# Kernel tuning notes

Hardware: AMD Instinct MI355X
Metric: run time of the kernel (lower is better)

Reference implementation:

```python
import jax, jax.numpy as jnp
import numpy as np

B, S, H = 2, 2048, 1024
I = 1024          # moe_intermediate_size
E = 8             # n_routed_experts
K = 2             # num_experts_per_tok
SCALE = 1.0       # routed_scaling_factor


def setup_inputs() -> dict:
    key = jax.random.key(0)
    ks = jax.random.split(key, 8)
    sd = 1.0 / np.sqrt(H)
    si = 1.0 / np.sqrt(I)
    return {
        "hidden_states": jax.random.normal(ks[0], (B, S, H), jnp.float32),
        "router_w": jax.random.uniform(ks[1], (E, H), jnp.float32, -sd, sd),
        # shared expert (n_shared_experts = 1); weights stored [in, out]
        "shared_gate": jax.random.uniform(ks[2], (H, I), jnp.float32, -sd, sd),
        "shared_up": jax.random.uniform(ks[3], (H, I), jnp.float32, -sd, sd),
        "shared_down": jax.random.uniform(ks[4], (I, H), jnp.float32, -si, si),
        # routed experts, stacked [E, in, out]
        "experts_gate": jax.random.uniform(ks[5], (E, H, I), jnp.float32, -sd, sd),
        "experts_up": jax.random.uniform(ks[6], (E, H, I), jnp.float32, -sd, sd),
        "experts_down": jax.random.uniform(ks[7], (E, I, H), jnp.float32, -si, si),
    }


def reference(hidden_states, router_w, shared_gate, shared_up, shared_down,
              experts_gate, experts_up, experts_down):
    residual = hidden_states
    x = hidden_states.reshape(-1, H)                      # [T, H], T = B*S

    # shared expert (SwiGLU-ish: sigmoid(gate) * up)
    sg = x @ shared_gate
    su = x @ shared_up
    shared_out = (jax.nn.sigmoid(sg) * su) @ shared_down  # [T, H]

    # router: softmax over experts, greedy top-k
    logits = x @ router_w.T                               # [T, E]
    scores = jax.nn.softmax(logits.astype(jnp.float32), axis=-1)
    topk_w, topk_idx = jax.lax.top_k(scores, K)           # [T, K]
    topk_w = topk_w * SCALE

    # dense compute of ALL experts on all tokens (faithful to reference)
    g = jnp.einsum('th,ehi->tei', x, experts_gate)        # [T, E, I]
    u = jnp.einsum('th,ehi->tei', x, experts_up)
    hid = jax.nn.sigmoid(g) * u
    expert_outputs = jnp.einsum('tei,eih->teh', hid, experts_down)  # [T, E, H]

    # gather top-k expert outputs and combine
    selected = jnp.take_along_axis(expert_outputs, topk_idx[:, :, None], axis=1)  # [T, K, H]
    routed_out = (selected * topk_w[:, :, None]).sum(axis=1)                      # [T, H]

    out = residual + (shared_out + routed_out).reshape(B, S, H)
    return out
```

## Files before the change

### kernel.cpp

```cpp
#include <hip/hip_runtime.h>
#include <hip/hip_bf16.h>

#define T_TOK 4096
#define HDIM 1024
#define IDIM 1024
#define EDIM 8
#define HID_SHARED_BASE 8320

typedef __attribute__((ext_vector_type(8))) short bf16x8;
typedef __attribute__((ext_vector_type(4))) float f32x4;

static __device__ __forceinline__ unsigned short f2bf(float f) {
  union { float f; unsigned int u; } v; v.f = f;
  unsigned int u = v.u;
  unsigned int r = u + 0x7FFFu + ((u >> 16) & 1u);
  return (unsigned short)(r >> 16);
}

#define GLD16(g, l) __builtin_amdgcn_global_load_lds( \
    (const __attribute__((address_space(1))) void*)(g), \
    (__attribute__((address_space(3))) void*)(l), 16, 0, 0)

__global__ __launch_bounds__(256) void convert_x(const float4* __restrict__ x4,
                                                 ushort4* __restrict__ xb4,
                                                 float4* __restrict__ out4) {
  int i = blockIdx.x * 256 + threadIdx.x;
  float4 v = x4[i];
  out4[i] = v;
  ushort4 o;
  o.x = f2bf(v.x); o.y = f2bf(v.y); o.z = f2bf(v.z); o.w = f2bf(v.w);
  xb4[i] = o;
}

__global__ void zero_cnt(int* __restrict__ cnt) {
  if (threadIdx.x < 16) cnt[threadIdx.x] = 0;
}

struct SrcPtrs { const float* p[6]; };

__global__ __launch_bounds__(256) void transpose_all(SrcPtrs S,
                                                     unsigned short* __restrict__ dstBase) {
  __shared__ unsigned short t[64][72];
  const int z = blockIdx.z;
  const float* src; int dz;
  if (z == 0)      { src = S.p[0];                              dz = 8;  }
  else if (z == 1) { src = S.p[1];                              dz = 17; }
  else if (z == 2) { src = S.p[2];                              dz = 26; }
  else if (z < 11) { src = S.p[3] + (size_t)(z - 3)  * 1048576; dz = z - 3; }
  else if (z < 19) { src = S.p[4] + (size_t)(z - 11) * 1048576; dz = 9 + (z - 11); }
  else             { src = S.p[5] + (size_t)(z - 19) * 1048576; dz = 18 + (z - 19); }
  unsigned short* dst = dstBase + (size_t)dz * 1048576;

  const int r0 = blockIdx.y * 64;
  const int c0 = blockIdx.x * 64;
  const int tid = threadIdx.x;

  const int rr = tid >> 4;
  const int c4 = (tid & 15) * 4;
#pragma unroll
  for (int ph = 0; ph < 4; ph++) {
    const int r = rr + ph * 16;
    const float4 v = *(const float4*)&src[(size_t)(r0 + r) * 1024 + c0 + c4];
    const int cs = c4 ^ (4 * (r >> 3));
    t[r][cs + 0] = f2bf(v.x); t[r][cs + 1] = f2bf(v.y);
    t[r][cs + 2] = f2bf(v.z); t[r][cs + 3] = f2bf(v.w);
  }
  __syncthreads();

  const int n = tid >> 3;
  const int k8 = (tid & 7) * 8;
  const int m = k8 >> 3;
#pragma unroll
  for (int ph = 0; ph < 2; ph++) {
    const int nn = n + ph * 32;
    const int ns = nn ^ (4 * m);
    unsigned short v[8];
#pragma unroll
    for (int j = 0; j < 8; j++) v[j] = t[k8 + j][ns];
    *(bf16x8*)&dst[(size_t)(c0 + nn) * 1024 + r0 + k8] = *(const bf16x8*)v;
  }
}

__global__ __launch_bounds__(256) void router2(
    const float* __restrict__ x, const float* __restrict__ rw,
    int* __restrict__ cnt, int* __restrict__ list, float* __restrict__ wgt) {
  __shared__ float rwT[1024 * 8];
  const int tid = threadIdx.x;
#pragma unroll
  for (int c = 0; c < 4; c++) {
    const int h = c * 256 + tid;
    float v[8];
#pragma unroll
    for (int e = 0; e < EDIM; e++) v[e] = rw[e * 1024 + h];
    *(float4*)&rwT[h * 8]     = make_float4(v[0], v[1], v[2], v[3]);
    *(float4*)&rwT[h * 8 + 4] = make_float4(v[4], v[5], v[6], v[7]);
  }
  __syncthreads();

  const int tt = tid >> 4;
  const int pp = tid & 15;
  const int t = blockIdx.x * 16 + tt;
  const float* xr = x + (size_t)t * HDIM;

  float a[EDIM];
#pragma unroll
  for (int e = 0; e < EDIM; e++) a[e] = 0.f;

#pragma unroll 8
  for (int i = 0; i < 64; i++) {
    const int h = pp + 16 * i;
    const float xs = xr[h];
    const float4 r0 = *(const float4*)&rwT[h * 8];
    const float4 r1 = *(const float4*)&rwT[h * 8 + 4];
    a[0] += xs * r0.x; a[1] += xs * r0.y; a[2] += xs * r0.z; a[3] += xs * r0.w;
    a[4] += xs * r1.x; a[5] += xs * r1.y; a[6] += xs * r1.z; a[7] += xs * r1.w;
  }
#pragma unroll
  for (int s = 1; s < 16; s <<= 1) {
#pragma unroll
    for (int e = 0; e < EDIM; e++) a[e] += __shfl_xor(a[e], s, 16);
  }
  if (pp == 0) {
    float m = a[0];
#pragma unroll
    for (int e = 1; e < EDIM; e++) m = fmaxf(m, a[e]);
    float p[EDIM]; float s = 0.f;
#pragma unroll
    for (int e = 0; e < EDIM; e++) { p[e] = expf(a[e] - m); s += p[e]; }
    float inv = 1.f / s;
    int e1 = 0; float b1 = p[0];
#pragma unroll
    for (int e = 1; e < EDIM; e++) if (p[e] > b1) { b1 = p[e]; e1 = e; }
    int e2 = -1; float b2 = -1.f;
#pragma unroll
    for (int e = 0; e < EDIM; e++) if (e != e1 && p[e] > b2) { b2 = p[e]; e2 = e; }
    int pos1 = atomicAdd(&cnt[e1], 1);
    list[e1 * T_TOK + pos1] = t; wgt[e1 * T_TOK + pos1] = b1 * inv;
    int pos2 = atomicAdd(&cnt[e2], 1);
    list[e2 * T_TOK + pos2] = t; wgt[e2 * T_TOK + pos2] = b2 * inv;
  }
}

__global__ __launch_bounds__(256) void gateup_f(
    const unsigned short* __restrict__ xb,
    const unsigned short* __restrict__ gateT,
    const unsigned short* __restrict__ upT,
    unsigned short* __restrict__ hid,
    const int* __restrict__ cnt, const int* __restrict__ list) {
  __shared__ unsigned short Al[3][128 * 32];
  __shared__ unsigned short Bg[3][64 * 32];
  __shared__ unsigned short Bu[3][64 * 32];

  const int tid = threadIdx.x;
  const int lane = tid & 63;
  const int w = tid >> 6;
  const int wm = w >> 1, wn = w & 1;
  const int z = blockIdx.z;
  const int m0 = blockIdx.y * 128;
  const int n0 = blockIdx.x * 64;

  int count, hidbase;
  if (z < EDIM) {
    count = cnt[z];
    if (m0 >= count) return;
    int off = 0;
#pragma unroll
    for (int i = 0; i < EDIM; i++) off += (i < z) ? cnt[i] : 0;
    hidbase = off;
  } else {
    count = T_TOK;
    hidbase = HID_SHARED_BASE;
  }
  const unsigned short* wg = gateT + (size_t)z * HDIM * IDIM;
  const unsigned short* wu = upT   + (size_t)z * HDIM * IDIM;

  const unsigned short* gA[2];
#pragma unroll
  for (int j = 0; j < 2; j++) {
    const int s = w * 128 + j * 64 + lane;
    const int row = s >> 2;
    const int g = (s & 3) ^ ((row + (row >> 2)) & 3);
    int tok;
    if (z < EDIM) {
      int p = m0 + row; if (p >= count) p = count - 1;
      tok = list[z * T_TOK + p];
    } else tok = m0 + row;
    gA[j] = xb + (size_t)tok * HDIM + g * 8;
  }
  const int sB = w * 64 + lane;
  const int rowB = sB >> 2;
  const int gB = (sB & 3) ^ ((rowB + (rowB >> 2)) & 3);
  const unsigned short* gGp = wg + (size_t)(n0 + rowB) * HDIM + gB * 8;
  const unsigned short* gUp = wu + (size_t)(n0 + rowB) * HDIM + gB * 8;

  f32x4 accg[4][2], accu[4][2];
  const f32x4 z4 = {0.f, 0.f, 0.f, 0.f};
#pragma unroll
  for (int i = 0; i < 4; i++)
#pragma unroll
    for (int j = 0; j < 2; j++) { accg[i][j] = z4; accu[i][j] = z4; }

  const int q = lane >> 4;
  const int r16 = lane & 15;
  const int ch = (q ^ ((r16 + (r16 >> 2)) & 3)) * 8;

  auto stage = [&](int k0, int b) {
    GLD16(gA[0] + k0, &Al[b][(w * 128) * 8]);
    GLD16(gA[1] + k0, &Al[b][(w * 128 + 64) * 8]);
    GLD16(gGp + k0, &Bg[b][(w * 64) * 8]);
    GLD16(gUp + k0, &Bu[b][(w * 64) * 8]);
  };
  auto compute = [&](int b) {
    bf16x8 af[4], bg2[2], bu2[2];
#pragma unroll
    for (int i = 0; i < 4; i++)
      af[i] = *(const bf16x8*)&Al[b][(wm * 64 + i * 16 + r16) * 32 + ch];
#pragma unroll
    for (int j = 0; j < 2; j++) {
      bg2[j] = *(const bf16x8*)&Bg[b][(wn * 32 + j * 16 + r16) * 32 + ch];
      bu2[j] = *(const bf16x8*)&Bu[b][(wn * 32 + j * 16 + r16) * 32 + ch];
    }
#pragma unroll
    for (int i = 0; i < 4; i++)
#pragma unroll
      for (int j = 0; j < 2; j++) {
        accg[i][j] = __builtin_amdgcn_mfma_f32_16x16x32_bf16(af[i], bg2[j], accg[i][j], 0, 0, 0);
        accu[i][j] = __builtin_amdgcn_mfma_f32_16x16x32_bf16(af[i], bu2[j], accu[i][j], 0, 0, 0);
      }
  };

  stage(0, 0);
  stage(32, 1);
#pragma unroll 1
  for (int p = 0; p < 32; p++) {
    if (p < 30) {
      asm volatile("s_waitcnt vmcnt(4)" ::: "memory");
    } else {
      asm volatile("s_waitcnt vmcnt(0)" ::: "memory");
    }
    __builtin_amdgcn_s_barrier();
    if (p + 2 < 32) stage((p + 2) * 32, (p + 2) % 3);
    compute(p % 3);
  }

#pragma unroll
  for (int i = 0; i < 4; i++) {
#pragma unroll
    for (int j = 0; j < 2; j++) {
      const int col = n0 + wn * 32 + j * 16 + r16;
#pragma unroll
      for (int r = 0; r < 4; r++) {
        int pos = m0 + wm * 64 + i * 16 + q * 4 + r;
        if (pos < count) {
          float g = accg[i][j][r], u = accu[i][j][r];
          float h = u / (1.f + __expf(-g));
          hid[(size_t)(hidbase + pos) * IDIM + col] = f2bf(h);
        }
      }
    }
  }
}

__global__ __launch_bounds__(256) void down_f(
    const unsigned short* __restrict__ hid,
    const unsigned short* __restrict__ downT,
    float* __restrict__ out,
    const int* __restrict__ cnt, const int* __restrict__ list,
    const float* __restrict__ wgt) {
  __shared__ unsigned short Al[3][128 * 32];
  __shared__ unsigned short Bl[3][128 * 32];

  const int tid = threadIdx.x;
  const int lane = tid & 63;
  const int w = tid >> 6;
  const int wm = w >> 1, wn = w & 1;
  const int z = blockIdx.z;
  const int m0 = blockIdx.y * 128;
  const int n0 = blockIdx.x * 128;

  int count, abase;
  if (z < EDIM) {
    count = cnt[z];
    if (m0 >= count) return;
    int off = 0;
#pragma unroll
    for (int i = 0; i < EDIM; i++) off += (i < z) ? cnt[i] : 0;
    abase = off;
  } else {
    count = T_TOK;
    abase = HID_SHARED_BASE;
  }
  const unsigned short* wd = downT + (size_t)z * IDIM * HDIM;

  const unsigned short *gA[2], *gBp[2];
#pragma unroll
  for (int j = 0; j < 2; j++) {
    const int s = w * 128 + j * 64 + lane;
    const int row = s >> 2;
    const int g = (s & 3) ^ ((row + (row >> 2)) & 3);
    gA[j]  = hid + (size_t)(abase + m0 + row) * IDIM + g * 8;
    gBp[j] = wd + (size_t)(n0 + row) * IDIM + g * 8;
  }

  f32x4 acc[4][4];
  const f32x4 z4 = {0.f, 0.f, 0.f, 0.f};
#pragma unroll
  for (int i = 0; i < 4; i++)
#pragma unroll
    for (int j = 0; j < 4; j++) acc[i][j] = z4;

  const int q = lane >> 4;
  const int r16 = lane & 15;
  const int ch = (q ^ ((r16 + (r16 >> 2)) & 3)) * 8;

  auto stage = [&](int k0, int b) {
    GLD16(gA[0] + k0,  &Al[b][(w * 128) * 8]);
    GLD16(gA[1] + k0,  &Al[b][(w * 128 + 64) * 8]);
    GLD16(gBp[0] + k0, &Bl[b][(w * 128) * 8]);
    GLD16(gBp[1] + k0, &Bl[b][(w * 128 + 64) * 8]);
  };
  auto compute = [&](int b) {
    bf16x8 af[4], bf4[4];
#pragma unroll
    for (int i = 0; i < 4; i++)
      af[i] = *(const bf16x8*)&Al[b][(wm * 64 + i * 16 + r16) * 32 + ch];
#pragma unroll
    for (int j = 0; j < 4; j++)
      bf4[j] = *(const bf16x8*)&Bl[b][(wn * 64 + j * 16 + r16) * 32 + ch];
#pragma unroll
    for (int i = 0; i < 4; i++)
#pragma unroll
      for (int j = 0; j < 4; j++)
        acc[i][j] = __builtin_amdgcn_mfma_f32_16x16x32_bf16(af[i], bf4[j], acc[i][j], 0, 0, 0);
  };

  stage(0, 0);
  stage(32, 1);
#pragma unroll 1
  for (int p = 0; p < 32; p++) {
    if (p < 30) {
      asm volatile("s_waitcnt vmcnt(4)" ::: "memory");
    } else {
      asm volatile("s_waitcnt vmcnt(0)" ::: "memory");
    }
    __builtin_amdgcn_s_barrier();
    if (p + 2 < 32) stage((p + 2) * 32, (p + 2) % 3);
    compute(p % 3);
  }

#pragma unroll
  for (int i = 0; i < 4; i++) {
    int toks[4]; float ws4[4];
#pragma unroll
    for (int r = 0; r < 4; r++) {
      int pos = m0 + wm * 64 + i * 16 + q * 4 + r;
      if (z < EDIM) {
        bool ok = pos < count;
        toks[r] = ok ? list[z * T_TOK + pos] : -1;
        ws4[r] = ok ? wgt[z * T_TOK + pos] : 0.f;
      } else {
        toks[r] = pos; ws4[r] = 1.f;
      }
    }
#pragma unroll
    for (int j = 0; j < 4; j++) {
      const int col = n0 + wn * 64 + j * 16 + r16;
#pragma unroll
      for (int r = 0; r < 4; r++) {
        if (toks[r] >= 0)
          atomicAdd(&out[(size_t)toks[r] * HDIM + col], ws4[r] * acc[i][j][r]);
      }
    }
  }
}

extern "C" void kernel_launch(void* const* d_in, const int* in_sizes, int n_in,
                              void* d_out, int out_size, void* d_ws, size_t ws_size,
                              hipStream_t stream) {
  const float* x  = (const float*)d_in[0];
  const float* rw = (const float*)d_in[1];
  const float* sg = (const float*)d_in[2];
  const float* su = (const float*)d_in[3];
  const float* sd = (const float*)d_in[4];
  const float* eg = (const float*)d_in[5];
  const float* eu = (const float*)d_in[6];
  const float* ed = (const float*)d_in[7];
  float* out = (float*)d_out;

  char* ws = (char*)d_ws;
  unsigned short* xb  = (unsigned short*)ws;
  unsigned short* hid = xb + (size_t)T_TOK * HDIM;
  int*   cnt  = (int*)(hid + (size_t)(HID_SHARED_BASE + T_TOK) * IDIM);
  int*   list = cnt + 16;
  float* wgt  = (float*)(list + EDIM * T_TOK);
  unsigned short* wT    = (unsigned short*)(wgt + EDIM * T_TOK);
  unsigned short* gateT = wT;
  unsigned short* upT   = wT + (size_t)9 * 1048576;
  unsigned short* downT = wT + (size_t)18 * 1048576;

  zero_cnt<<<1, 64, 0, stream>>>(cnt);
  convert_x<<<(T_TOK * HDIM) / 1024, 256, 0, stream>>>(
      (const float4*)x, (ushort4*)xb, (float4*)out);
  router2<<<T_TOK / 16, 256, 0, stream>>>(x, rw, cnt, list, wgt);

  SrcPtrs S; S.p[0] = sg; S.p[1] = su; S.p[2] = sd; S.p[3] = eg; S.p[4] = eu; S.p[5] = ed;
  transpose_all<<<dim3(16, 16, 27), 256, 0, stream>>>(S, wT);

  gateup_f<<<dim3(IDIM / 64, 32, 9), 256, 0, stream>>>(xb, gateT, upT, hid, cnt, list);
  down_f<<<dim3(HDIM / 128, 32, 9), 256, 0, stream>>>(hid, downT, out, cnt, list, wgt);
}
```

Measured before the change: 378.5 us.

## Replace atomic output accumulation with bf16 staging buffer, register transpose, fused zeroing

Adds a workspace buffer R with three bf16 slots per token (two routed experts plus the shared expert). down_f writes its weighted results there instead of issuing float atomicAdds into the output, and a new combine kernel sums the slots with the residual. The weight transpose now works in registers without shared memory, and zeroing the counters is folded into convert_x so one launch is dropped. This removes atomic contention and the extra output initialisation pass, at the cost of bf16 rounding of partial outputs, extra memory traffic for R, and a dependence on the workspace being large enough.

```diff
diff --git a/kernel.cpp b/kernel.cpp
--- a/kernel.cpp
+++ b/kernel.cpp
@@ -16,6 +16,10 @@
   unsigned int r = u + 0x7FFFu + ((u >> 16) & 1u);
   return (unsigned short)(r >> 16);
 }
+static __device__ __forceinline__ float bf2f(unsigned short s) {
+  union { unsigned int u; float f; } v; v.u = ((unsigned int)s) << 16;
+  return v.f;
+}
 
 #define GLD16(g, l) __builtin_amdgcn_global_load_lds( \
     (const __attribute__((address_space(1))) void*)(g), \
@@ -23,24 +27,21 @@
 
 __global__ __launch_bounds__(256) void convert_x(const float4* __restrict__ x4,
                                                  ushort4* __restrict__ xb4,
-                                                 float4* __restrict__ out4) {
+                                                 float4* __restrict__ out4,
+                                                 int* __restrict__ cnt, int initOut) {
   int i = blockIdx.x * 256 + threadIdx.x;
+  if (blockIdx.x == 0 && threadIdx.x < 16) cnt[threadIdx.x] = 0;
   float4 v = x4[i];
-  out4[i] = v;
+  if (initOut) out4[i] = v;
   ushort4 o;
   o.x = f2bf(v.x); o.y = f2bf(v.y); o.z = f2bf(v.z); o.w = f2bf(v.w);
   xb4[i] = o;
 }
 
-__global__ void zero_cnt(int* __restrict__ cnt) {
-  if (threadIdx.x < 16) cnt[threadIdx.x] = 0;
-}
-
 struct SrcPtrs { const float* p[6]; };
 
 __global__ __launch_bounds__(256) void transpose_all(SrcPtrs S,
                                                      unsigned short* __restrict__ dstBase) {
-  __shared__ unsigned short t[64][72];
   const int z = blockIdx.z;
   const float* src; int dz;
   if (z == 0)      { src = S.p[0];                              dz = 8;  }
@@ -51,33 +52,25 @@
   else             { src = S.p[5] + (size_t)(z - 19) * 1048576; dz = 18 + (z - 19); }
   unsigned short* dst = dstBase + (size_t)dz * 1048576;
 
-  const int r0 = blockIdx.y * 64;
-  const int c0 = blockIdx.x * 64;
   const int tid = threadIdx.x;
-
-  const int rr = tid >> 4;
-  const int c4 = (tid & 15) * 4;
-#pragma unroll
-  for (int ph = 0; ph < 4; ph++) {
-    const int r = rr + ph * 16;
-    const float4 v = *(const float4*)&src[(size_t)(r0 + r) * 1024 + c0 + c4];
-    const int cs = c4 ^ (4 * (r >> 3));
-    t[r][cs + 0] = f2bf(v.x); t[r][cs + 1] = f2bf(v.y);
-    t[r][cs + 2] = f2bf(v.z); t[r][cs + 3] = f2bf(v.w);
-  }
-  __syncthreads();
-
-  const int n = tid >> 3;
-  const int k8 = (tid & 7) * 8;
-  const int m = k8 >> 3;
-#pragma unroll
-  for (int ph = 0; ph < 2; ph++) {
-    const int nn = n + ph * 32;
-    const int ns = nn ^ (4 * m);
-    unsigned short v[8];
-#pragma unroll
-    for (int j = 0; j < 8; j++) v[j] = t[k8 + j][ns];
-    *(bf16x8*)&dst[(size_t)(c0 + nn) * 1024 + r0 + k8] = *(const bf16x8*)v;
+  const int rid = tid & 7;
+  const int cid = tid >> 3;
+  const int r = blockIdx.y * 64 + rid * 8;
+  const int c = blockIdx.x * 128 + cid * 4;
+
+  float4 v[8];
+#pragma unroll
+  for (int i = 0; i < 8; i++)
+    v[i] = *(const float4*)&src[(size_t)(r + i) * 1024 + c];
+
+#pragma unroll
+  for (int j = 0; j < 4; j++) {
+    unsigned short o[8];
+    o[0] = f2bf(v[0][j]); o[1] = f2bf(v[1][j]);
+    o[2] = f2bf(v[2][j]); o[3] = f2bf(v[3][j]);
+    o[4] = f2bf(v[4][j]); o[5] = f2bf(v[5][j]);
+    o[6] = f2bf(v[6][j]); o[7] = f2bf(v[7][j]);
+    *(bf16x8*)&dst[(size_t)(c + j) * 1024 + r] = *(const bf16x8*)o;
   }
 }
 
@@ -135,9 +128,9 @@
 #pragma unroll
     for (int e = 0; e < EDIM; e++) if (e != e1 && p[e] > b2) { b2 = p[e]; e2 = e; }
     int pos1 = atomicAdd(&cnt[e1], 1);
-    list[e1 * T_TOK + pos1] = t; wgt[e1 * T_TOK + pos1] = b1 * inv;
+    list[e1 * T_TOK + pos1] = (t << 1);      wgt[e1 * T_TOK + pos1] = b1 * inv;
     int pos2 = atomicAdd(&cnt[e2], 1);
-    list[e2 * T_TOK + pos2] = t; wgt[e2 * T_TOK + pos2] = b2 * inv;
+    list[e2 * T_TOK + pos2] = (t << 1) | 1;  wgt[e2 * T_TOK + pos2] = b2 * inv;
   }
 }
 
@@ -183,7 +176,7 @@
     int tok;
     if (z < EDIM) {
       int p = m0 + row; if (p >= count) p = count - 1;
-      tok = list[z * T_TOK + p];
+      tok = list[z * T_TOK + p] >> 1;
     } else tok = m0 + row;
     gA[j] = xb + (size_t)tok * HDIM + g * 8;
   }
@@ -264,7 +257,7 @@
 __global__ __launch_bounds__(256) void down_f(
     const unsigned short* __restrict__ hid,
     const unsigned short* __restrict__ downT,
-    float* __restrict__ out,
+    float* __restrict__ out, unsigned short* __restrict__ R, int useR,
     const int* __restrict__ cnt, const int* __restrict__ list,
     const float* __restrict__ wgt) {
   __shared__ unsigned short Al[3][128 * 32];
@@ -350,16 +343,17 @@
 
 #pragma unroll
   for (int i = 0; i < 4; i++) {
-    int toks[4]; float ws4[4];
+    int toks[4]; int slot[4]; float ws4[4];
 #pragma unroll
     for (int r = 0; r < 4; r++) {
       int pos = m0 + wm * 64 + i * 16 + q * 4 + r;
       if (z < EDIM) {
         bool ok = pos < count;
-        toks[r] = ok ? list[z * T_TOK + pos] : -1;
+        int v = ok ? list[z * T_TOK + pos] : -2;
+        toks[r] = v >> 1; slot[r] = v & 1;
         ws4[r] = ok ? wgt[z * T_TOK + pos] : 0.f;
       } else {
-        toks[r] = pos; ws4[r] = 1.f;
+        toks[r] = pos; slot[r] = 2; ws4[r] = 1.f;
       }
     }
 #pragma unroll
@@ -367,11 +361,40 @@
       const int col = n0 + wn * 64 + j * 16 + r16;
 #pragma unroll
       for (int r = 0; r < 4; r++) {
-        if (toks[r] >= 0)
-          atomicAdd(&out[(size_t)toks[r] * HDIM + col], ws4[r] * acc[i][j][r]);
+        if (toks[r] >= 0) {
+          float v = ws4[r] * acc[i][j][r];
+          if (useR) {
+            R[((size_t)toks[r] * 3 + slot[r]) * HDIM + col] = f2bf(v);
+          } else {
+            atomicAdd(&out[(size_t)toks[r] * HDIM + col], v);
+          }
+        }
       }
     }
   }
+}
+
+__global__ __launch_bounds__(256) void combine_k(const float4* __restrict__ x4,
+                                                 const unsigned short* __restrict__ R,
+                                                 float4* __restrict__ out4) {
+  const int i8 = blockIdx.x * 256 + threadIdx.x;
+  const int t = i8 >> 7;
+  const int c8 = (i8 & 127) * 8;
+  const unsigned short* r0 = R + ((size_t)t * 3) * 1024 + c8;
+  float s[8];
+#pragma unroll
+  for (int k = 0; k < 8; k++) s[k] = 0.f;
+#pragma unroll
+  for (int sl = 0; sl < 3; sl++) {
+    bf16x8 v = *(const bf16x8*)(r0 + sl * 1024);
+#pragma unroll
+    for (int k = 0; k < 8; k++) s[k] += bf2f(((const unsigned short*)&v)[k]);
+  }
+  float4 a = x4[i8 * 2], b = x4[i8 * 2 + 1];
+  a.x += s[0]; a.y += s[1]; a.z += s[2]; a.w += s[3];
+  b.x += s[4]; b.y += s[5]; b.z += s[6]; b.w += s[7];
+  out4[i8 * 2] = a;
+  out4[i8 * 2 + 1] = b;
 }
 
 extern "C" void kernel_launch(void* const* d_in, const int* in_sizes, int n_in,
@@ -397,15 +420,22 @@
   unsigned short* gateT = wT;
   unsigned short* upT   = wT + (size_t)9 * 1048576;
   unsigned short* downT = wT + (size_t)18 * 1048576;
-
-  zero_cnt<<<1, 64, 0, stream>>>(cnt);
+  unsigned short* R = wT + (size_t)27 * 1048576;
+  size_t need = ((char*)(R + (size_t)T_TOK * 3 * HDIM)) - ws;
+  const int useR = (ws_size >= need) ? 1 : 0;
+
   convert_x<<<(T_TOK * HDIM) / 1024, 256, 0, stream>>>(
-      (const float4*)x, (ushort4*)xb, (float4*)out);
+      (const float4*)x, (ushort4*)xb, (float4*)out, cnt, useR ? 0 : 1);
   router2<<<T_TOK / 16, 256, 0, stream>>>(x, rw, cnt, list, wgt);
 
   SrcPtrs S; S.p[0] = sg; S.p[1] = su; S.p[2] = sd; S.p[3] = eg; S.p[4] = eu; S.p[5] = ed;
-  transpose_all<<<dim3(16, 16, 27), 256, 0, stream>>>(S, wT);
+  transpose_all<<<dim3(8, 16, 27), 256, 0, stream>>>(S, wT);
 
   gateup_f<<<dim3(IDIM / 64, 32, 9), 256, 0, stream>>>(xb, gateT, upT, hid, cnt, list);
-  down_f<<<dim3(HDIM / 128, 32, 9), 256, 0, stream>>>(hid, downT, out, cnt, list, wgt);
-}
+  down_f<<<dim3(HDIM / 128, 32, 9), 256, 0, stream>>>(hid, downT, out, R, useR,
+                                                      cnt, list, wgt);
+  if (useR) {
+    combine_k<<<(T_TOK * HDIM / 8) / 256, 256, 0, stream>>>(
+        (const float4*)x, R, (float4*)out);
+  }
+}
```

Result: no change. 378.4 us (-0.0%).
